# Optimization experiments

Hardware: AMD Instinct MI355X
Metric: run time of the kernel (lower is better)

Reference implementation:

```python
import jax, jax.numpy as jnp
import numpy as np

# Mixtral-style config (scaled)
L = 2          # num_hidden_layers
H = 1024       # hidden_size
NH = 16        # num_attention_heads
KVH = 4        # num_key_value_heads
HD = H // NH   # head_dim = 64
F = 1024       # intermediate_size (per expert)
E = 8          # num_local_experts
K = 2          # num_experts_per_tok
EPS = 1e-5     # rms_norm_eps
THETA = 1e6    # rope_theta
B, S = 1, 2048


def setup_inputs() -> dict:
    key = jax.random.key(0)
    ks = jax.random.split(key, 10)
    s = 0.02
    inputs_embeds = jax.random.normal(ks[0], (B, S, H), jnp.float32)
    ln1 = jnp.ones((L, H), jnp.float32)
    ln2 = jnp.ones((L, H), jnp.float32)
    final_ln = jnp.ones((H,), jnp.float32)
    q_w = jax.random.normal(ks[1], (L, NH * HD, H), jnp.float32) * s
    k_w = jax.random.normal(ks[2], (L, KVH * HD, H), jnp.float32) * s
    v_w = jax.random.normal(ks[3], (L, KVH * HD, H), jnp.float32) * s
    o_w = jax.random.normal(ks[4], (L, H, NH * HD), jnp.float32) * s
    gate_w = jax.random.normal(ks[5], (L, E, H), jnp.float32) * s
    w1 = jax.random.normal(ks[6], (L, E, F, H), jnp.float32) * s
    w2 = jax.random.normal(ks[7], (L, E, H, F), jnp.float32) * s
    w3 = jax.random.normal(ks[8], (L, E, F, H), jnp.float32) * s
    return {"inputs_embeds": inputs_embeds, "ln1": ln1, "ln2": ln2,
            "final_ln": final_ln, "q_w": q_w, "k_w": k_w, "v_w": v_w,
            "o_w": o_w, "gate_w": gate_w, "w1": w1, "w2": w2, "w3": w3}


def _rmsnorm(x, w):
    v = jnp.mean(jnp.square(x), axis=-1, keepdims=True)
    return (x * jax.lax.rsqrt(v + EPS)) * w


def _rotate_half(x):
    x1, x2 = jnp.split(x, 2, axis=-1)
    return jnp.concatenate([-x2, x1], axis=-1)


def _rope_tables():
    inv_freq = 1.0 / (THETA ** (jnp.arange(0, HD, 2, dtype=jnp.float32) / HD))
    t = jnp.arange(S, dtype=jnp.float32)
    freqs = jnp.outer(t, inv_freq)              # [S, HD/2]
    emb = jnp.concatenate([freqs, freqs], -1)   # [S, HD]
    return jnp.cos(emb), jnp.sin(emb)


def _attn(x, qw, kw, vw, ow, cos, sin, mask):
    q = (x @ qw.T).reshape(B, S, NH, HD).transpose(0, 2, 1, 3)    # [B,NH,S,D]
    k = (x @ kw.T).reshape(B, S, KVH, HD).transpose(0, 2, 1, 3)   # [B,KVH,S,D]
    v = (x @ vw.T).reshape(B, S, KVH, HD).transpose(0, 2, 1, 3)
    q = q * cos + _rotate_half(q) * sin
    k = k * cos + _rotate_half(k) * sin
    rep = NH // KVH
    k = jnp.repeat(k, rep, axis=1)   # GQA expand -> [B,NH,S,D]
    v = jnp.repeat(v, rep, axis=1)
    scores = jnp.einsum('bhqd,bhkd->bhqk', q, k) / jnp.sqrt(jnp.float32(HD))
    scores = jnp.where(mask, scores, jnp.finfo(scores.dtype).min)
    p = jax.nn.softmax(scores, axis=-1)
    o = jnp.einsum('bhqk,bhkd->bhqd', p, v)
    o = o.transpose(0, 2, 1, 3).reshape(B, S, NH * HD)
    return o @ ow.T


def _moe(x, gw, w1_l, w2_l, w3_l):
    xf = x.reshape(-1, H)                                   # [T,H]
    T = xf.shape[0]
    logits = xf @ gw.T                                      # [T,E]
    probs = jax.nn.softmax(logits, axis=-1)
    topw, topi = jax.lax.top_k(probs, K)                    # [T,K]
    topw = topw / jnp.sum(topw, axis=-1, keepdims=True)
    wfull = jnp.zeros((T, E), probs.dtype).at[jnp.arange(T)[:, None], topi].set(topw)
    g = jnp.einsum('th,efh->tef', xf, w1_l)                 # [T,E,F]
    u = jnp.einsum('th,efh->tef', xf, w3_l)
    a = jax.nn.silu(g) * u
    y = jnp.einsum('te,tef,ehf->th', wfull, a, w2_l)
    return y.reshape(x.shape)


def reference(inputs_embeds, ln1, ln2, final_ln, q_w, k_w, v_w, o_w, gate_w, w1, w2, w3):
    cos, sin = _rope_tables()
    mask = jnp.tril(jnp.ones((S, S), bool))[None, None]     # causal
    h = inputs_embeds
    for l in range(L):
        h = h + _attn(_rmsnorm(h, ln1[l]), q_w[l], k_w[l], v_w[l], o_w[l], cos, sin, mask)
        h = h + _moe(_rmsnorm(h, ln2[l]), gate_w[l], w1[l], w2[l], w3[l])
    return _rmsnorm(h, final_ln)
```

## Files before the change

kernel.cpp:

```cpp
#include <hip/hip_runtime.h>
#include <hip/hip_bf16.h>
#include <math.h>

#define S_LEN 2048
#define HID   1024
#define NHEAD 16
#define KVH   4
#define HD    64
#define FF    1024
#define NE    8
#define NL    2

#define OFF_H    0
#define OFF_Q    (OFF_H + S_LEN*HID)
#define OFF_K    (OFF_Q + S_LEN*HID)
#define OFF_V    (OFF_K + S_LEN*KVH*HD)
#define OFF_COS  (OFF_V + S_LEN*KVH*HD)
#define OFF_SIN  (OFF_COS + S_LEN*32)
#define OFF_WT   (OFF_SIN + S_LEN*32)
#define OFF_INT  (OFF_WT + NE*S_LEN)
#define OFF_TOPE (OFF_INT + NE*S_LEN + 16)
#define OFF_TOPW (OFF_TOPE + S_LEN)
#define OFF_XH   (OFF_TOPW + 2*S_LEN)
#define OFF_AOH  (OFF_XH + S_LEN*HID/2)
#define OFF_ABH  (OFF_AOH + S_LEN*HID/2)
#define OFF_Q16  (OFF_ABH + NE*S_LEN*FF/2)
#define OFF_K16  (OFF_Q16 + S_LEN*HID/2)
#define OFF_VT16 (OFF_K16 + S_LEN*KVH*HD/2)
#define OFF_PO   (OFF_VT16 + S_LEN*KVH*HD/2)
#define OFF_PM   (OFF_PO + 80*NHEAD*64*64)
#define OFF_PL   (OFF_PM + 80*NHEAD*64)
#define OFF_WCVT (OFF_PL + 80*NHEAD*64)

typedef __attribute__((ext_vector_type(8))) _Float16 f16x8;
typedef __attribute__((ext_vector_type(8))) short  s16x8;
typedef __attribute__((ext_vector_type(4))) float  f32x4;

__device__ __forceinline__ short f2h(float f) {
    union { _Float16 h; short s; } u;
    u.h = (_Float16)f;
    return u.s;
}

__device__ __forceinline__ s16x8 cvt8(float4 a, float4 b) {
    s16x8 w;
    w[0]=f2h(a.x); w[1]=f2h(a.y); w[2]=f2h(a.z); w[3]=f2h(a.w);
    w[4]=f2h(b.x); w[5]=f2h(b.y); w[6]=f2h(b.z); w[7]=f2h(b.w);
    return w;
}

__global__ __launch_bounds__(256) void cvt16_kernel(const float* __restrict__ src,
                                                    short* __restrict__ dst, int n8) {
    int gid = blockIdx.x * 256 + threadIdx.x;
    if (gid >= n8) return;
    const float4* s = (const float4*)src + (size_t)gid * 2;
    *(s16x8*)(dst + (size_t)gid * 8) = cvt8(s[0], s[1]);
}

__global__ void rope_tables_kernel(float* __restrict__ cosb, float* __restrict__ sinb) {
    int gid = blockIdx.x * 256 + threadIdx.x;
    int t = gid >> 5, i = gid & 31;
    float invf = powf(1.0e6f, -(float)i / 32.0f);
    float ang = (float)t * invf;
    cosb[gid] = cosf(ang);
    sinb[gid] = sinf(ang);
}

__global__ __launch_bounds__(256) void rmsnorm_h16_kernel(const float* __restrict__ x,
                                                          const float* __restrict__ w,
                                                          short* __restrict__ oh) {
    int row = blockIdx.x;
    const float4* xr = (const float4*)(x + (size_t)row * HID);
    float4 xv = xr[threadIdx.x];
    float ss = xv.x*xv.x + xv.y*xv.y + xv.z*xv.z + xv.w*xv.w;
    for (int off = 32; off; off >>= 1) ss += __shfl_xor(ss, off);
    __shared__ float sred[4];
    if ((threadIdx.x & 63) == 0) sred[threadIdx.x >> 6] = ss;
    __syncthreads();
    float tot = sred[0] + sred[1] + sred[2] + sred[3];
    float scale = rsqrtf(tot * (1.0f / (float)HID) + 1e-5f);
    float4 wv = ((const float4*)w)[threadIdx.x];
    float4 o;
    o.x = xv.x * scale * wv.x; o.y = xv.y * scale * wv.y;
    o.z = xv.z * scale * wv.z; o.w = xv.w * scale * wv.w;
    union { short s[4]; float2 f2; } hh;
    hh.s[0]=f2h(o.x); hh.s[1]=f2h(o.y); hh.s[2]=f2h(o.z); hh.s[3]=f2h(o.w);
    ((float2*)(oh + (size_t)row * HID))[threadIdx.x] = hh.f2;
}

__global__ __launch_bounds__(256) void rmsnorm_gate_kernel(const float* __restrict__ x,
                                                           const float* __restrict__ w,
                                                           const float* __restrict__ gw,
                                                           short* __restrict__ oh,
                                                           int* __restrict__ tope,
                                                           float2* __restrict__ topw) {
    int row = blockIdx.x;
    const float4* xr = (const float4*)(x + (size_t)row * HID);
    float4 xv = xr[threadIdx.x];
    float ss = xv.x*xv.x + xv.y*xv.y + xv.z*xv.z + xv.w*xv.w;
    for (int off = 32; off; off >>= 1) ss += __shfl_xor(ss, off);
    __shared__ float sred[4];
    __shared__ float gred[4][NE];
    if ((threadIdx.x & 63) == 0) sred[threadIdx.x >> 6] = ss;
    __syncthreads();
    float tot = sred[0] + sred[1] + sred[2] + sred[3];
    float scale = rsqrtf(tot * (1.0f / (float)HID) + 1e-5f);
    float4 wv = ((const float4*)w)[threadIdx.x];
    float4 o;
    o.x = xv.x * scale * wv.x; o.y = xv.y * scale * wv.y;
    o.z = xv.z * scale * wv.z; o.w = xv.w * scale * wv.w;
    union { short s[4]; float2 f2; } hh;
    hh.s[0]=f2h(o.x); hh.s[1]=f2h(o.y); hh.s[2]=f2h(o.z); hh.s[3]=f2h(o.w);
    ((float2*)(oh + (size_t)row * HID))[threadIdx.x] = hh.f2;
    const float4* gr = (const float4*)gw;
    float acc[NE];
    #pragma unroll
    for (int e = 0; e < NE; ++e) {
        float4 g4 = gr[e * 256 + threadIdx.x];
        acc[e] = o.x*g4.x + o.y*g4.y + o.z*g4.z + o.w*g4.w;
    }
    #pragma unroll
    for (int e = 0; e < NE; ++e)
        for (int off = 32; off; off >>= 1) acc[e] += __shfl_xor(acc[e], off);
    if ((threadIdx.x & 63) == 0) {
        #pragma unroll
        for (int e = 0; e < NE; ++e) gred[threadIdx.x >> 6][e] = acc[e];
    }
    __syncthreads();
    if (threadIdx.x == 0) {
        float lg[NE];
        #pragma unroll
        for (int e = 0; e < NE; ++e)
            lg[e] = gred[0][e] + gred[1][e] + gred[2][e] + gred[3][e];
        float mx = lg[0];
        #pragma unroll
        for (int e = 1; e < NE; ++e) mx = fmaxf(mx, lg[e]);
        float p[NE];
        #pragma unroll
        for (int e = 0; e < NE; ++e) p[e] = __expf(lg[e] - mx);
        int i0 = 0;
        #pragma unroll
        for (int e = 1; e < NE; ++e) if (p[e] > p[i0]) i0 = e;
        int i1 = -1;
        #pragma unroll
        for (int e = 0; e < NE; ++e) if (e != i0 && (i1 < 0 || p[e] > p[i1])) i1 = e;
        float w0 = p[i0], w1 = p[i1];
        float inv = 1.0f / (w0 + w1);
        tope[row] = i0 | (i1 << 8);
        topw[row] = make_float2(w0 * inv, w1 * inv);
    }
}

__global__ __launch_bounds__(1024) void route_build_kernel(const int* __restrict__ tope,
                                                           const float2* __restrict__ topw,
                                                           int* __restrict__ cnt,
                                                           int* __restrict__ idx,
                                                           float* __restrict__ wt) {
    const int e = blockIdx.x;
    const int lane = threadIdx.x & 63, wv = threadIdx.x >> 6;
    __shared__ int wtot[16];
    __shared__ int sbase;
    if (threadIdx.x == 0) sbase = 0;
    __syncthreads();
    for (int t0 = 0; t0 < S_LEN; t0 += 1024) {
        int t = t0 + threadIdx.x;
        int pk = tope[t];
        int e0 = pk & 0xff, e1 = (pk >> 8) & 0xff;
        bool sel = (e0 == e) || (e1 == e);
        unsigned long long mask = __ballot(sel);
        int prefix = __popcll(mask & ((1ULL << lane) - 1ULL));
        if (lane == 0) wtot[wv] = __popcll(mask);
        __syncthreads();
        if (sel) {
            int off = sbase;
            for (int i = 0; i < wv; ++i) off += wtot[i];
            float2 wpair = topw[t];
            float wsel = (e0 == e) ? wpair.x : wpair.y;
            int slot = off + prefix;
            idx[e * S_LEN + slot] = t;
            wt[e * S_LEN + slot] = wsel;
        }
        __syncthreads();
        if (threadIdx.x == 0) {
            int s = 0;
            #pragma unroll
            for (int i = 0; i < 16; ++i) s += wtot[i];
            sbase += s;
        }
    }
    __syncthreads();
    if (threadIdx.x == 0) cnt[e] = sbase;
}

__global__ __launch_bounds__(256) void rmsnorm_kernel(const float* __restrict__ x,
                                                      const float* __restrict__ w,
                                                      float* __restrict__ out) {
    int row = blockIdx.x;
    const float4* xr = (const float4*)(x + (size_t)row * HID);
    float4 xv = xr[threadIdx.x];
    float ss = xv.x*xv.x + xv.y*xv.y + xv.z*xv.z + xv.w*xv.w;
    for (int off = 32; off; off >>= 1) ss += __shfl_xor(ss, off);
    __shared__ float sred[4];
    if ((threadIdx.x & 63) == 0) sred[threadIdx.x >> 6] = ss;
    __syncthreads();
    float tot = sred[0] + sred[1] + sred[2] + sred[3];
    float scale = rsqrtf(tot * (1.0f / (float)HID) + 1e-5f);
    float4 wv = ((const float4*)w)[threadIdx.x];
    float4 o;
    o.x = xv.x * scale * wv.x; o.y = xv.y * scale * wv.y;
    o.z = xv.z * scale * wv.z; o.w = xv.w * scale * wv.w;
    ((float4*)(out + (size_t)row * HID))[threadIdx.x] = o;
}

__global__ void rope_cvt_kernel(const float* __restrict__ p, const float* __restrict__ cosb,
                                const float* __restrict__ sinb, short* __restrict__ o16,
                                int nh, int total) {
    int gid = blockIdx.x * 256 + threadIdx.x;
    if (gid >= total) return;
    int per = nh * 32;
    int t = gid / per, r = gid % per;
    int hh = r >> 5, i = r & 31;
    float c = cosb[t*32 + i], s = sinb[t*32 + i];
    const float* base = p + (size_t)t * (nh * HD) + hh * HD + i;
    float a = base[0], b = base[32];
    short* ob = o16 + (size_t)t * (nh * HD) + hh * HD + i;
    ob[0]  = f2h(a * c - b * s);
    ob[32] = f2h(b * c + a * s);
}

__global__ __launch_bounds__(256) void vtrans_kernel(const float* __restrict__ vb,
                                                     short* __restrict__ vt16) {
    __shared__ float tile[64][65];
    const int t0 = blockIdx.x * 64, d0 = blockIdx.y * 64;
    const int tr = threadIdx.x >> 2;
    const int dc = (threadIdx.x & 3) * 16;
    const float4* src = (const float4*)(vb + (size_t)(t0 + tr) * (KVH*HD) + d0 + dc);
    float4 v0 = src[0], v1 = src[1], v2 = src[2], v3 = src[3];
    tile[tr][dc+ 0]=v0.x; tile[tr][dc+ 1]=v0.y; tile[tr][dc+ 2]=v0.z; tile[tr][dc+ 3]=v0.w;
    tile[tr][dc+ 4]=v1.x; tile[tr][dc+ 5]=v1.y; tile[tr][dc+ 6]=v1.z; tile[tr][dc+ 7]=v1.w;
    tile[tr][dc+ 8]=v2.x; tile[tr][dc+ 9]=v2.y; tile[tr][dc+10]=v2.z; tile[tr][dc+11]=v2.w;
    tile[tr][dc+12]=v3.x; tile[tr][dc+13]=v3.y; tile[tr][dc+14]=v3.z; tile[tr][dc+15]=v3.w;
    __syncthreads();
    const int dr = threadIdx.x >> 2;
    const int tc = (threadIdx.x & 3) * 16;
    s16x8 w0, w1;
    #pragma unroll
    for (int i = 0; i < 8; ++i) {
        w0[i] = f2h(tile[tc + i][dr]);
        w1[i] = f2h(tile[tc + 8 + i][dr]);
    }
    short* dst = vt16 + (size_t)(d0 + dr) * S_LEN + t0 + tc;
    *(s16x8*)dst = w0;
    *(s16x8*)(dst + 8) = w1;
}

__device__ __forceinline__ void gemm64_core(
        const short* pA0, const short* pB0, const short* pB1,
        int Kd, int tid, short* As, short* Bs, f32x4 (&acc)[2][4]) {
    const int lane = tid & 63, lo = lane & 15, hi = lane >> 4;
    const int wid = tid >> 6, wr = wid >> 1, wc = wid & 1;
    const int srow = tid >> 2, scol = (tid & 3) * 8;
    s16x8 a0 = *(const s16x8*)pA0;
    s16x8 b0 = *(const s16x8*)pB0;
    s16x8 b1 = *(const s16x8*)pB1;
    *(s16x8*)&As[srow*40 + scol] = a0;
    *(s16x8*)&Bs[srow*40 + scol] = b0;
    *(s16x8*)&Bs[(64+srow)*40 + scol] = b1;
    __syncthreads();
    int p = 0;
    for (int k0 = 0; k0 < Kd; k0 += 32) {
        const bool more = (k0 + 32 < Kd);
        if (more) {
            a0 = *(const s16x8*)(pA0 + k0 + 32);
            b0 = *(const s16x8*)(pB0 + k0 + 32);
            b1 = *(const s16x8*)(pB1 + k0 + 32);
        }
        const short* Asp = As + p * (64*40);
        const short* Bsp = Bs + p * (128*40);
        f16x8 aF[2], bF[4];
        #pragma unroll
        for (int m = 0; m < 2; ++m) aF[m] = *(const f16x8*)&Asp[(wr*32 + m*16 + lo)*40 + hi*8];
        #pragma unroll
        for (int n = 0; n < 4; ++n) bF[n] = *(const f16x8*)&Bsp[(wc*64 + n*16 + lo)*40 + hi*8];
        #pragma unroll
        for (int m = 0; m < 2; ++m)
            #pragma unroll
            for (int n = 0; n < 4; ++n)
                acc[m][n] = __builtin_amdgcn_mfma_f32_16x16x32_f16(aF[m], bF[n], acc[m][n], 0, 0, 0);
        if (more) {
            short* Asn = As + (p ^ 1) * (64*40);
            short* Bsn = Bs + (p ^ 1) * (128*40);
            *(s16x8*)&Asn[srow*40 + scol] = a0;
            *(s16x8*)&Bsn[srow*40 + scol] = b0;
            *(s16x8*)&Bsn[(64+srow)*40 + scol] = b1;
        }
        __syncthreads();
        p ^= 1;
    }
}

__global__ __launch_bounds__(256) void gemm_h16_kernel(const short* __restrict__ Ag,
        const short* __restrict__ Bg, float* __restrict__ C,
        const float* __restrict__ resid, int N, int Kd) {
    __shared__ __align__(16) short As[2*64*40], Bs[2*128*40];
    const int tid = threadIdx.x;
    const int lane = tid & 63, lo = lane & 15, hi = lane >> 4;
    const int wid = tid >> 6, wr = wid >> 1, wc = wid & 1;
    const int m0 = blockIdx.y * 64, n0 = blockIdx.x * 128;
    const int srow = tid >> 2, scol = (tid & 3) * 8;
    f32x4 acc[2][4];
    #pragma unroll
    for (int m = 0; m < 2; ++m)
        #pragma unroll
        for (int n = 0; n < 4; ++n) { acc[m][n][0]=0.f; acc[m][n][1]=0.f; acc[m][n][2]=0.f; acc[m][n][3]=0.f; }
    gemm64_core(Ag + (size_t)(m0+srow)*Kd + scol,
                Bg + (size_t)(n0+srow)*Kd + scol, Bg + (size_t)(n0+64+srow)*Kd + scol,
                Kd, tid, As, Bs, acc);
    #pragma unroll
    for (int m = 0; m < 2; ++m)
        #pragma unroll
        for (int n = 0; n < 4; ++n)
            #pragma unroll
            for (int r = 0; r < 4; ++r) {
                int row = m0 + wr*32 + m*16 + hi*4 + r;
                int col = n0 + wc*64 + n*16 + lo;
                float val = acc[m][n][r];
                if (resid) val += resid[(size_t)row * N + col];
                C[(size_t)row * N + col] = val;
            }
}

__global__ __launch_bounds__(256) void qkv_h16_kernel(const short* __restrict__ Xh,
        const short* __restrict__ qw16, const short* __restrict__ kw16,
        const short* __restrict__ vw16,
        float* __restrict__ qo, float* __restrict__ ko, float* __restrict__ vo) {
    __shared__ __align__(16) short As[2*64*40], Bs[2*128*40];
    const int bx = blockIdx.x;
    const short* Bp; float* Cp; int Nc, n0;
    if (bx < 8)       { Bp = qw16; Cp = qo; Nc = 1024; n0 = bx * 128; }
    else if (bx < 10) { Bp = kw16; Cp = ko; Nc = 256;  n0 = (bx - 8) * 128; }
    else              { Bp = vw16; Cp = vo; Nc = 256;  n0 = (bx - 10) * 128; }
    const int tid = threadIdx.x;
    const int lane = tid & 63, lo = lane & 15, hi = lane >> 4;
    const int wid = tid >> 6, wr = wid >> 1, wc = wid & 1;
    const int m0 = blockIdx.y * 64;
    const int srow = tid >> 2, scol = (tid & 3) * 8;
    f32x4 acc[2][4];
    #pragma unroll
    for (int m = 0; m < 2; ++m)
        #pragma unroll
        for (int n = 0; n < 4; ++n) { acc[m][n][0]=0.f; acc[m][n][1]=0.f; acc[m][n][2]=0.f; acc[m][n][3]=0.f; }
    gemm64_core(Xh + (size_t)(m0+srow)*HID + scol,
                Bp + (size_t)(n0+srow)*HID + scol, Bp + (size_t)(n0+64+srow)*HID + scol,
                HID, tid, As, Bs, acc);
    #pragma unroll
    for (int m = 0; m < 2; ++m)
        #pragma unroll
        for (int n = 0; n < 4; ++n)
            #pragma unroll
            for (int r = 0; r < 4; ++r) {
                int row = m0 + wr*32 + m*16 + hi*4 + r;
                int col = n0 + wc*64 + n*16 + lo;
                Cp[(size_t)row * Nc + col] = acc[m][n][r];
            }
}

__global__ __launch_bounds__(256) void attn_mfma_kernel(const short* __restrict__ q16,
                                                        const short* __restrict__ k16,
                                                        const short* __restrict__ vt16,
                                                        float* __restrict__ pO,
                                                        float* __restrict__ pm,
                                                        float* __restrict__ pl) {
    __shared__ __align__(16) short Ks[64][72];
    __shared__ __align__(16) short Vt[64][72];
    __shared__ __align__(16) short Ps[4][16][72];
    const int wid = threadIdx.x >> 6, lane = threadIdx.x & 63;
    const int lo = lane & 15, hi = lane >> 4;
    const int head = blockIdx.y;
    const int s = 79 - blockIdx.x;
    int qi, c;
    if (s < 8)       { qi = s;                     c = 0; }
    else if (s < 24) { int t = s - 8;  qi = 8  + (t >> 1); c = t & 1; }
    else if (s < 48) { int t = s - 24; qi = 16 + t / 3;    c = t % 3; }
    else             { int t = s - 48; qi = 24 + (t >> 2); c = t & 3; }
    const int t_beg = c * 8;
    const int t_end = min(t_beg + 8, qi + 1);
    const int q0 = qi * 64;
    const int kvh = head >> 2;

    f16x8 qf[2];
    {
        const short* qr = q16 + (size_t)(q0 + wid*16 + lo) * HID + head*HD;
        qf[0] = *(const f16x8*)(qr + hi*8);
        qf[1] = *(const f16x8*)(qr + 32 + hi*8);
    }

    f32x4 acc[4];
    float m[4], l[4];
    #pragma unroll
    for (int r = 0; r < 4; ++r) {
        m[r] = -1e30f; l[r] = 0.f;
        acc[0][r] = 0.f; acc[1][r] = 0.f; acc[2][r] = 0.f; acc[3][r] = 0.f;
    }

    const int skey = threadIdx.x >> 2;
    const int sdg  = (threadIdx.x & 3) * 16;

    s16x8 ka0, ka1, va0, va1;
    {
        const short* kr = k16 + (size_t)(t_beg*64 + skey)*(KVH*HD) + kvh*HD + sdg;
        ka0 = *(const s16x8*)kr; ka1 = *(const s16x8*)(kr + 8);
        const short* vr = vt16 + (size_t)(kvh*HD + skey)*S_LEN + t_beg*64 + sdg;
        va0 = *(const s16x8*)vr; va1 = *(const s16x8*)(vr + 8);
    }

    for (int t = t_beg; t < t_end; ++t) {
        __syncthreads();
        *(s16x8*)&Ks[skey][sdg]     = ka0;
        *(s16x8*)&Ks[skey][sdg + 8] = ka1;
        *(s16x8*)&Vt[skey][sdg]     = va0;
        *(s16x8*)&Vt[skey][sdg + 8] = va1;
        __syncthreads();
        if (t + 1 < t_end) {
            const short* kr = k16 + (size_t)((t+1)*64 + skey)*(KVH*HD) + kvh*HD + sdg;
            ka0 = *(const s16x8*)kr; ka1 = *(const s16x8*)(kr + 8);
            const short* vr = vt16 + (size_t)(kvh*HD + skey)*S_LEN + (t+1)*64 + sdg;
            va0 = *(const s16x8*)vr; va1 = *(const s16x8*)(vr + 8);
        }
        const int k0 = t * 64;
        f32x4 sc[4];
        #pragma unroll
        for (int f = 0; f < 4; ++f) {
            f32x4 sf; sf[0]=0.f; sf[1]=0.f; sf[2]=0.f; sf[3]=0.f;
            f16x8 bk0 = *(const f16x8*)&Ks[f*16 + lo][hi*8];
            sf = __builtin_amdgcn_mfma_f32_16x16x32_f16(qf[0], bk0, sf, 0, 0, 0);
            f16x8 bk1 = *(const f16x8*)&Ks[f*16 + lo][32 + hi*8];
            sf = __builtin_amdgcn_mfma_f32_16x16x32_f16(qf[1], bk1, sf, 0, 0, 0);
            sc[f] = sf;
        }
        #pragma unroll
        for (int f = 0; f < 4; ++f)
            #pragma unroll
            for (int r = 0; r < 4; ++r) sc[f][r] *= 0.125f;
        if (t == qi) {
            int qrow = q0 + wid*16 + hi*4;
            #pragma unroll
            for (int f = 0; f < 4; ++f)
                #pragma unroll
                for (int r = 0; r < 4; ++r)
                    if (k0 + f*16 + lo > qrow + r) sc[f][r] = -1e30f;
        }
        float scale_[4];
        #pragma unroll
        for (int r = 0; r < 4; ++r) {
            float x = fmaxf(fmaxf(sc[0][r], sc[1][r]), fmaxf(sc[2][r], sc[3][r]));
            x = fmaxf(x, __shfl_xor(x, 1));
            x = fmaxf(x, __shfl_xor(x, 2));
            x = fmaxf(x, __shfl_xor(x, 4));
            x = fmaxf(x, __shfl_xor(x, 8));
            float mn = fmaxf(m[r], x);
            scale_[r] = __expf(m[r] - mn);
            m[r] = mn;
            l[r] *= scale_[r];
            acc[0][r] *= scale_[r]; acc[1][r] *= scale_[r];
            acc[2][r] *= scale_[r]; acc[3][r] *= scale_[r];
        }
        float rs[4] = {0.f, 0.f, 0.f, 0.f};
        #pragma unroll
        for (int f = 0; f < 4; ++f)
            #pragma unroll
            for (int r = 0; r < 4; ++r) {
                float e = __expf(sc[f][r] - m[r]);
                rs[r] += e;
                Ps[wid][hi*4 + r][f*16 + lo] = f2h(e);
            }
        #pragma unroll
        for (int r = 0; r < 4; ++r) {
            float x = rs[r];
            x += __shfl_xor(x, 1); x += __shfl_xor(x, 2);
            x += __shfl_xor(x, 4); x += __shfl_xor(x, 8);
            l[r] += x;
        }
        asm volatile("s_waitcnt lgkmcnt(0)" ::: "memory");
        __builtin_amdgcn_sched_barrier(0);
        f16x8 pa0 = *(const f16x8*)&Ps[wid][lo][hi*8];
        f16x8 pa1 = *(const f16x8*)&Ps[wid][lo][32 + hi*8];
        #pragma unroll
        for (int f = 0; f < 4; ++f) {
            f32x4 o = acc[f];
            f16x8 v0 = *(const f16x8*)&Vt[f*16 + lo][hi*8];
            o = __builtin_amdgcn_mfma_f32_16x16x32_f16(pa0, v0, o, 0, 0, 0);
            f16x8 v1 = *(const f16x8*)&Vt[f*16 + lo][32 + hi*8];
            o = __builtin_amdgcn_mfma_f32_16x16x32_f16(pa1, v1, o, 0, 0, 0);
            acc[f] = o;
        }
    }
    const int pbase = head * 80 + s;
    float* po = pO + (size_t)pbase * 4096;
    #pragma unroll
    for (int r = 0; r < 4; ++r)
        #pragma unroll
        for (int f = 0; f < 4; ++f)
            po[(wid*16 + hi*4 + r) * 64 + f*16 + lo] = acc[f][r];
    if (lo == 0) {
        #pragma unroll
        for (int r = 0; r < 4; ++r) {
            pm[pbase*64 + wid*16 + hi*4 + r] = m[r];
            pl[pbase*64 + wid*16 + hi*4 + r] = l[r];
        }
    }
}

__global__ __launch_bounds__(256) void attn_combine_kernel(const float* __restrict__ pO,
        const float* __restrict__ pm, const float* __restrict__ pl,
        short* __restrict__ aoh) {
    const int qi = blockIdx.x, head = blockIdx.y;
    const int nch = qi / 8 + 1;
    int sbase;
    if (qi < 8)       sbase = qi;
    else if (qi < 16) sbase = 8 + (qi - 8) * 2;
    else if (qi < 24) sbase = 24 + (qi - 16) * 3;
    else              sbase = 48 + (qi - 24) * 4;
    const int row = threadIdx.x >> 2;
    const int d0 = (threadIdx.x & 3) * 16;
    float mv[4], lv[4];
    float mx = -1e30f;
    #pragma unroll
    for (int cd = 0; cd < 4; ++cd) {
        if (cd < nch) {
            int p = head * 80 + sbase + cd;
            mv[cd] = pm[p * 64 + row];
            lv[cd] = pl[p * 64 + row];
            mx = fmaxf(mx, mv[cd]);
        } else { mv[cd] = -1e30f; lv[cd] = 0.f; }
    }
    float w[4];
    float lsum = 0.f;
    #pragma unroll
    for (int cd = 0; cd < 4; ++cd) {
        w[cd] = (cd < nch) ? __expf(mv[cd] - mx) : 0.f;
        lsum += w[cd] * lv[cd];
    }
    float inv = 1.0f / lsum;
    float o[16] = {};
    #pragma unroll
    for (int cd = 0; cd < 4; ++cd) {
        if (cd < nch) {
            const float4* po = (const float4*)(pO + ((size_t)(head * 80 + sbase + cd)) * 4096 + row * 64 + d0);
            float wc = w[cd] * inv;
            #pragma unroll
            for (int j = 0; j < 4; ++j) {
                float4 vv = po[j];
                o[j*4+0] += wc * vv.x; o[j*4+1] += wc * vv.y;
                o[j*4+2] += wc * vv.z; o[j*4+3] += wc * vv.w;
            }
        }
    }
    size_t outb = (size_t)(qi * 64 + row) * HID + head * HD + d0;
    s16x8 w0, w1;
    #pragma unroll
    for (int i = 0; i < 8; ++i) { w0[i] = f2h(o[i]); w1[i] = f2h(o[8+i]); }
    *(s16x8*)(aoh + outb) = w0;
    *(s16x8*)(aoh + outb + 8) = w1;
}

__global__ __launch_bounds__(256) void moe_mlp1_h16(const short* __restrict__ Xh,
        const short* __restrict__ W1h, const short* __restrict__ W3h,
        const int* __restrict__ cnt, const int* __restrict__ idx,
        short* __restrict__ abh) {
    int e = blockIdx.z;
    int ne = cnt[e];
    int m0 = blockIdx.y * 64;
    if (m0 >= ne) return;
    int f0 = blockIdx.x * 64;
    __shared__ __align__(16) short As[2*64*40];
    __shared__ __align__(16) short Gs[2*64*40], Us[2*64*40];
    __shared__ int rows[64];
    const int tid = threadIdx.x;
    if (tid < 64) {
        int slot = m0 + tid;
        rows[tid] = (slot < ne) ? idx[e * S_LEN + slot] : 0;
    }
    __syncthreads();
    const int lane = tid & 63, lo = lane & 15, hi = lane >> 4;
    const int wid = tid >> 6, wr = wid >> 1, wc = wid & 1;
    const int srow = tid >> 2, scol = (tid & 3) * 8;
    const short* pX0 = Xh + (size_t)rows[srow] * HID + scol;
    const short* p1 = W1h + ((size_t)e * FF + f0 + srow) * HID + scol;
    const short* p3 = W3h + ((size_t)e * FF + f0 + srow) * HID + scol;

    f32x4 ag[2][2], au[2][2];
    #pragma unroll
    for (int m = 0; m < 2; ++m)
        #pragma unroll
        for (int n = 0; n < 2; ++n) {
            ag[m][n][0]=0.f; ag[m][n][1]=0.f; ag[m][n][2]=0.f; ag[m][n][3]=0.f;
            au[m][n][0]=0.f; au[m][n][1]=0.f; au[m][n][2]=0.f; au[m][n][3]=0.f;
        }

    s16x8 a0 = *(const s16x8*)pX0;
    s16x8 g0 = *(const s16x8*)p1;
    s16x8 u0 = *(const s16x8*)p3;
    *(s16x8*)&As[srow*40 + scol] = a0;
    *(s16x8*)&Gs[srow*40 + scol] = g0;
    *(s16x8*)&Us[srow*40 + scol] = u0;
    __syncthreads();
    int p = 0;
    for (int k0 = 0; k0 < HID; k0 += 32) {
        const bool more = (k0 + 32 < HID);
        if (more) {
            a0 = *(const s16x8*)(pX0 + k0 + 32);
            g0 = *(const s16x8*)(p1 + k0 + 32);
            u0 = *(const s16x8*)(p3 + k0 + 32);
        }
        const short* Asp = As + p * (64*40);
        const short* Gsp = Gs + p * (64*40);
        const short* Usp = Us + p * (64*40);
        f16x8 aF[2], gF[2], uF[2];
        #pragma unroll
        for (int m = 0; m < 2; ++m) aF[m] = *(const f16x8*)&Asp[(wr*32 + m*16 + lo)*40 + hi*8];
        #pragma unroll
        for (int n = 0; n < 2; ++n) {
            gF[n] = *(const f16x8*)&Gsp[(wc*32 + n*16 + lo)*40 + hi*8];
            uF[n] = *(const f16x8*)&Usp[(wc*32 + n*16 + lo)*40 + hi*8];
        }
        #pragma unroll
        for (int m = 0; m < 2; ++m)
            #pragma unroll
            for (int n = 0; n < 2; ++n) {
                ag[m][n] = __builtin_amdgcn_mfma_f32_16x16x32_f16(aF[m], gF[n], ag[m][n], 0, 0, 0);
                au[m][n] = __builtin_amdgcn_mfma_f32_16x16x32_f16(aF[m], uF[n], au[m][n], 0, 0, 0);
            }
        if (more) {
            short* Asn = As + (p ^ 1) * (64*40);
            short* Gsn = Gs + (p ^ 1) * (64*40);
            short* Usn = Us + (p ^ 1) * (64*40);
            *(s16x8*)&Asn[srow*40 + scol] = a0;
            *(s16x8*)&Gsn[srow*40 + scol] = g0;
            *(s16x8*)&Usn[srow*40 + scol] = u0;
        }
        __syncthreads();
        p ^= 1;
    }
    #pragma unroll
    for (int m = 0; m < 2; ++m)
        #pragma unroll
        for (int n = 0; n < 2; ++n)
            #pragma unroll
            for (int r = 0; r < 4; ++r) {
                int slot = m0 + wr*32 + m*16 + hi*4 + r;
                if (slot >= ne) continue;
                float g = ag[m][n][r], u = au[m][n][r];
                float a = g * (1.0f / (1.0f + __expf(-g))) * u;
                abh[((size_t)e * S_LEN + slot) * FF + f0 + wc*32 + n*16 + lo] = f2h(a);
            }
}

__global__ __launch_bounds__(256) void moe_mlp2_h16(const short* __restrict__ abh,
        const short* __restrict__ W2h,
        const int* __restrict__ cnt, const int* __restrict__ idx,
        const float* __restrict__ wt, float* __restrict__ hbuf) {
    int e = blockIdx.z;
    int ne = cnt[e];
    int m0 = blockIdx.y * 64;
    if (m0 >= ne) return;
    int n0 = blockIdx.x * 128;
    __shared__ __align__(16) short As[2*64*40], Bs[2*128*40];
    const int tid = threadIdx.x;
    const int lane = tid & 63, lo = lane & 15, hi = lane >> 4;
    const int wid = tid >> 6, wr = wid >> 1, wc = wid & 1;
    const int srow = tid >> 2, scol = (tid & 3) * 8;
    f32x4 acc[2][4];
    #pragma unroll
    for (int m = 0; m < 2; ++m)
        #pragma unroll
        for (int n = 0; n < 4; ++n) { acc[m][n][0]=0.f; acc[m][n][1]=0.f; acc[m][n][2]=0.f; acc[m][n][3]=0.f; }
    gemm64_core(abh + ((size_t)e*S_LEN + m0 + srow)*FF + scol,
                W2h + ((size_t)e*HID + n0 + srow)*FF + scol,
                W2h + ((size_t)e*HID + n0 + 64 + srow)*FF + scol,
                FF, tid, As, Bs, acc);
    #pragma unroll
    for (int m = 0; m < 2; ++m) {
        #pragma unroll
        for (int r = 0; r < 4; ++r) {
            int slot = m0 + wr*32 + m*16 + hi*4 + r;
            if (slot >= ne) continue;
            int tok = idx[e * S_LEN + slot];
            float wv = wt[e * S_LEN + slot];
            #pragma unroll
            for (int n = 0; n < 4; ++n)
                atomicAdd(&hbuf[(size_t)tok * HID + n0 + wc*64 + n*16 + lo], acc[m][n][r] * wv);
        }
    }
}

extern "C" void kernel_launch(void* const* d_in, const int* in_sizes, int n_in,
                              void* d_out, int out_size, void* d_ws, size_t ws_size,
                              hipStream_t stream) {
    const float* emb = (const float*)d_in[0];
    const float* ln1 = (const float*)d_in[1];
    const float* ln2 = (const float*)d_in[2];
    const float* fln = (const float*)d_in[3];
    const float* qw  = (const float*)d_in[4];
    const float* kw  = (const float*)d_in[5];
    const float* vw  = (const float*)d_in[6];
    const float* ow  = (const float*)d_in[7];
    const float* gw  = (const float*)d_in[8];
    const float* w1  = (const float*)d_in[9];
    const float* w2  = (const float*)d_in[10];
    const float* w3  = (const float*)d_in[11];

    float* ws   = (float*)d_ws;
    float* h    = ws + OFF_H;
    float* q    = ws + OFF_Q;
    float* kb   = ws + OFF_K;
    float* vb   = ws + OFF_V;
    float* cosb = ws + OFF_COS;
    float* sinb = ws + OFF_SIN;
    float* wt   = ws + OFF_WT;
    int*   cnt  = (int*)(ws + OFF_INT);
    int*   idx  = cnt + 8;
    int*   tope = (int*)(ws + OFF_TOPE);
    float2* topw = (float2*)(ws + OFF_TOPW);
    short* xh   = (short*)(ws + OFF_XH);
    short* aoh  = (short*)(ws + OFF_AOH);
    short* abh  = (short*)(ws + OFF_ABH);
    short* q16  = (short*)(ws + OFF_Q16);
    short* k16  = (short*)(ws + OFF_K16);
    short* vt16 = (short*)(ws + OFF_VT16);
    float* pO   = ws + OFF_PO;
    float* pm   = ws + OFF_PM;
    float* pl   = ws + OFF_PL;
    short* WC   = (short*)(ws + OFF_WCVT);

    short* sq = WC;
    short* sk = sq + HID*HID;
    short* sv = sk + KVH*HD*HID;
    short* so = sv + KVH*HD*HID;
    short* s1 = so + HID*HID;
    short* s3 = s1 + (size_t)NE*FF*HID;
    short* s2 = s3 + (size_t)NE*FF*HID;

    hipMemcpyAsync(h, emb, (size_t)S_LEN * HID * sizeof(float), hipMemcpyDeviceToDevice, stream);
    rope_tables_kernel<<<S_LEN * 32 / 256, 256, 0, stream>>>(cosb, sinb);

    const int n8_qo = HID*HID/8, n8_kv = KVH*HD*HID/8, n8_w = NE*FF*HID/8;

    for (int l = 0; l < NL; ++l) {
        cvt16_kernel<<<n8_qo/256, 256, 0, stream>>>(qw + (size_t)l*HID*HID, sq, n8_qo);
        cvt16_kernel<<<n8_kv/256, 256, 0, stream>>>(kw + (size_t)l*KVH*HD*HID, sk, n8_kv);
        cvt16_kernel<<<n8_kv/256, 256, 0, stream>>>(vw + (size_t)l*KVH*HD*HID, sv, n8_kv);
        cvt16_kernel<<<n8_qo/256, 256, 0, stream>>>(ow + (size_t)l*HID*HID, so, n8_qo);

        rmsnorm_h16_kernel<<<S_LEN, 256, 0, stream>>>(h, ln1 + l * HID, xh);
        qkv_h16_kernel<<<dim3(12, 32), 256, 0, stream>>>(xh, sq, sk, sv, q, kb, vb);
        rope_cvt_kernel<<<(S_LEN * NHEAD * 32) / 256, 256, 0, stream>>>(q, cosb, sinb, q16, NHEAD, S_LEN * NHEAD * 32);
        rope_cvt_kernel<<<(S_LEN * KVH * 32) / 256, 256, 0, stream>>>(kb, cosb, sinb, k16, KVH, S_LEN * KVH * 32);
        vtrans_kernel<<<dim3(S_LEN/64, KVH*HD/64), 256, 0, stream>>>(vb, vt16);
        attn_mfma_kernel<<<dim3(80, NHEAD), 256, 0, stream>>>(q16, k16, vt16, pO, pm, pl);
        attn_combine_kernel<<<dim3(32, NHEAD), 256, 0, stream>>>(pO, pm, pl, aoh);
        gemm_h16_kernel<<<dim3(8, 32), 256, 0, stream>>>(aoh, so, h, h, HID, HID);

        rmsnorm_gate_kernel<<<S_LEN, 256, 0, stream>>>(h, ln2 + l * HID, gw + (size_t)l * NE * HID,
                                                       xh, tope, topw);
        route_build_kernel<<<NE, 1024, 0, stream>>>(tope, topw, cnt, idx, wt);

        cvt16_kernel<<<n8_w/256, 256, 0, stream>>>(w1 + (size_t)l*NE*FF*HID, s1, n8_w);
        cvt16_kernel<<<n8_w/256, 256, 0, stream>>>(w3 + (size_t)l*NE*FF*HID, s3, n8_w);
        moe_mlp1_h16<<<dim3(16, 32, 8), 256, 0, stream>>>(xh, s1, s3, cnt, idx, abh);

        cvt16_kernel<<<n8_w/256, 256, 0, stream>>>(w2 + (size_t)l*NE*HID*FF, s2, n8_w);
        moe_mlp2_h16<<<dim3(8, 32, 8), 256, 0, stream>>>(abh, s2, cnt, idx, wt, h);
    }
    rmsnorm_kernel<<<S_LEN, 256, 0, stream>>>(h, fln, (float*)d_out);
}
```

Measured before the change: 490.5 us.

## Fold softmax scale into Q, lazy rescale in attention, split-K MoE down-proj

Moves the 1/sqrt(d) scale into the RoPE conversion of Q so the attention loop no longer multiplies the scores. Adds a lazy online-softmax rescale: the running max and accumulators are updated only when some row's tile max exceeds the stored max by more than 8, saving exp and multiply work on most tiles. The MoE second GEMM is split along K into two halves, doubling the grid, and both halves accumulate through the existing atomics. In exchange there are twice as many atomic adds, and the lazy rescale lets exponentials grow to about e^8, which is still fine for fp16 probabilities and fp32 sums.

Result: no change. 488.1 us (-0.5%).

```diff
diff --git a/kernel.cpp b/kernel.cpp
--- a/kernel.cpp
+++ b/kernel.cpp
@@ -214,7 +214,7 @@
 
 __global__ void rope_cvt_kernel(const float* __restrict__ p, const float* __restrict__ cosb,
                                 const float* __restrict__ sinb, short* __restrict__ o16,
-                                int nh, int total) {
+                                int nh, int total, float qscale) {
     int gid = blockIdx.x * 256 + threadIdx.x;
     if (gid >= total) return;
     int per = nh * 32;
@@ -224,8 +224,8 @@
     const float* base = p + (size_t)t * (nh * HD) + hh * HD + i;
     float a = base[0], b = base[32];
     short* ob = o16 + (size_t)t * (nh * HD) + hh * HD + i;
-    ob[0]  = f2h(a * c - b * s);
-    ob[32] = f2h(b * c + a * s);
+    ob[0]  = f2h((a * c - b * s) * qscale);
+    ob[32] = f2h((b * c + a * s) * qscale);
 }
 
 __global__ __launch_bounds__(256) void vtrans_kernel(const float* __restrict__ vb,
@@ -438,10 +438,6 @@
             sf = __builtin_amdgcn_mfma_f32_16x16x32_f16(qf[1], bk1, sf, 0, 0, 0);
             sc[f] = sf;
         }
-        #pragma unroll
-        for (int f = 0; f < 4; ++f)
-            #pragma unroll
-            for (int r = 0; r < 4; ++r) sc[f][r] *= 0.125f;
         if (t == qi) {
             int qrow = q0 + wid*16 + hi*4;
             #pragma unroll
@@ -450,7 +446,7 @@
                 for (int r = 0; r < 4; ++r)
                     if (k0 + f*16 + lo > qrow + r) sc[f][r] = -1e30f;
         }
-        float scale_[4];
+        float pmax[4];
         #pragma unroll
         for (int r = 0; r < 4; ++r) {
             float x = fmaxf(fmaxf(sc[0][r], sc[1][r]), fmaxf(sc[2][r], sc[3][r]));
@@ -458,12 +454,20 @@
             x = fmaxf(x, __shfl_xor(x, 2));
             x = fmaxf(x, __shfl_xor(x, 4));
             x = fmaxf(x, __shfl_xor(x, 8));
-            float mn = fmaxf(m[r], x);
-            scale_[r] = __expf(m[r] - mn);
-            m[r] = mn;
-            l[r] *= scale_[r];
-            acc[0][r] *= scale_[r]; acc[1][r] *= scale_[r];
-            acc[2][r] *= scale_[r]; acc[3][r] *= scale_[r];
+            pmax[r] = x;
+        }
+        bool ok = (pmax[0] <= m[0] + 8.f) && (pmax[1] <= m[1] + 8.f) &&
+                  (pmax[2] <= m[2] + 8.f) && (pmax[3] <= m[3] + 8.f);
+        if (!__all(ok)) {
+            #pragma unroll
+            for (int r = 0; r < 4; ++r) {
+                float mn = fmaxf(m[r], pmax[r]);
+                float sc_ = __expf(m[r] - mn);
+                m[r] = mn;
+                l[r] *= sc_;
+                acc[0][r] *= sc_; acc[1][r] *= sc_;
+                acc[2][r] *= sc_; acc[3][r] *= sc_;
+            }
         }
         float rs[4] = {0.f, 0.f, 0.f, 0.f};
         #pragma unroll
@@ -660,11 +664,13 @@
         const short* __restrict__ W2h,
         const int* __restrict__ cnt, const int* __restrict__ idx,
         const float* __restrict__ wt, float* __restrict__ hbuf) {
-    int e = blockIdx.z;
+    int e = blockIdx.z >> 1;
+    int ks = blockIdx.z & 1;
     int ne = cnt[e];
     int m0 = blockIdx.y * 64;
     if (m0 >= ne) return;
     int n0 = blockIdx.x * 128;
+    const int koff = ks * (FF / 2);
     __shared__ __align__(16) short As[2*64*40], Bs[2*128*40];
     const int tid = threadIdx.x;
     const int lane = tid & 63, lo = lane & 15, hi = lane >> 4;
@@ -675,10 +681,10 @@
     for (int m = 0; m < 2; ++m)
         #pragma unroll
         for (int n = 0; n < 4; ++n) { acc[m][n][0]=0.f; acc[m][n][1]=0.f; acc[m][n][2]=0.f; acc[m][n][3]=0.f; }
-    gemm64_core(abh + ((size_t)e*S_LEN + m0 + srow)*FF + scol,
-                W2h + ((size_t)e*HID + n0 + srow)*FF + scol,
-                W2h + ((size_t)e*HID + n0 + 64 + srow)*FF + scol,
-                FF, tid, As, Bs, acc);
+    gemm64_core(abh + ((size_t)e*S_LEN + m0 + srow)*FF + koff + scol,
+                W2h + ((size_t)e*HID + n0 + srow)*FF + koff + scol,
+                W2h + ((size_t)e*HID + n0 + 64 + srow)*FF + koff + scol,
+                FF / 2, tid, As, Bs, acc);
     #pragma unroll
     for (int m = 0; m < 2; ++m) {
         #pragma unroll
@@ -754,8 +760,8 @@
 
         rmsnorm_h16_kernel<<<S_LEN, 256, 0, stream>>>(h, ln1 + l * HID, xh);
         qkv_h16_kernel<<<dim3(12, 32), 256, 0, stream>>>(xh, sq, sk, sv, q, kb, vb);
-        rope_cvt_kernel<<<(S_LEN * NHEAD * 32) / 256, 256, 0, stream>>>(q, cosb, sinb, q16, NHEAD, S_LEN * NHEAD * 32);
-        rope_cvt_kernel<<<(S_LEN * KVH * 32) / 256, 256, 0, stream>>>(kb, cosb, sinb, k16, KVH, S_LEN * KVH * 32);
+        rope_cvt_kernel<<<(S_LEN * NHEAD * 32) / 256, 256, 0, stream>>>(q, cosb, sinb, q16, NHEAD, S_LEN * NHEAD * 32, 0.125f);
+        rope_cvt_kernel<<<(S_LEN * KVH * 32) / 256, 256, 0, stream>>>(kb, cosb, sinb, k16, KVH, S_LEN * KVH * 32, 1.0f);
         vtrans_kernel<<<dim3(S_LEN/64, KVH*HD/64), 256, 0, stream>>>(vb, vt16);
         attn_mfma_kernel<<<dim3(80, NHEAD), 256, 0, stream>>>(q16, k16, vt16, pO, pm, pl);
         attn_combine_kernel<<<dim3(32, NHEAD), 256, 0, stream>>>(pO, pm, pl, aoh);
@@ -770,7 +776,7 @@
         moe_mlp1_h16<<<dim3(16, 32, 8), 256, 0, stream>>>(xh, s1, s3, cnt, idx, abh);
 
         cvt16_kernel<<<n8_w/256, 256, 0, stream>>>(w2 + (size_t)l*NE*HID*FF, s2, n8_w);
-        moe_mlp2_h16<<<dim3(8, 32, 8), 256, 0, stream>>>(abh, s2, cnt, idx, wt, h);
+        moe_mlp2_h16<<<dim3(8, 32, 16), 256, 0, stream>>>(abh, s2, cnt, idx, wt, h);
     }
     rmsnorm_kernel<<<S_LEN, 256, 0, stream>>>(h, fln, (float*)d_out);
 }
```
